# Kernel tuning notes

Measured on AMD Instinct MI355X. Metric: run time of the kernel, lower is better.

Reference implementation:

```python
import jax, jax.numpy as jnp
import numpy as np
import math

B, LQ, LK = 4, 512, 512
D_MODEL, NHEAD, NLABELS = 512, 8, 8
D_Q = D_MODEL // NHEAD


def setup_inputs() -> dict:
    key = jax.random.key(0)
    ks = jax.random.split(key, 12)
    xavier = lambda k, shape: jax.random.uniform(
        k, shape, jnp.float32,
        -math.sqrt(6.0 / (shape[0] + shape[1])), math.sqrt(6.0 / (shape[0] + shape[1])))
    return {
        "q": jax.random.normal(ks[0], (B, LQ, D_MODEL), jnp.float32),
        "k": jax.random.normal(ks[1], (B, LK, D_MODEL), jnp.float32),
        "edge_mask": jax.random.randint(ks[2], (B, LQ, LK, NLABELS), 0, 2).astype(jnp.float32),
        "padding_mask": jax.random.randint(ks[3], (B, LQ, LK), 0, 2).astype(jnp.float32),
        "w_q_w": xavier(ks[4], (D_MODEL, D_MODEL)),
        "w_q_b": jnp.zeros((D_MODEL,), jnp.float32),
        "w_k": xavier(ks[5], (D_MODEL, D_MODEL)),
        "w_v": xavier(ks[6], (D_MODEL, D_MODEL)),
        "w_h_w": xavier(ks[7], (D_MODEL, D_MODEL)),
        "w_h_b": jnp.zeros((D_MODEL,), jnp.float32),
        "b_ks": xavier(ks[8], (NLABELS, D_Q)),
        "b_vs": xavier(ks[9], (NLABELS, D_Q)),
    }


def reference(q, k, edge_mask, padding_mask, w_q_w, w_q_b, w_k, w_v, w_h_w, w_h_b, b_ks, b_vs):
    sz_b, len_q, _ = q.shape
    len_k = k.shape[1]
    temp = np.power(D_Q, 0.5).astype(np.float32)

    # projections -> (nhead, B, L, d_q), matching torch permute(2,0,1,3)
    query = (q @ w_q_w.T + w_q_b).reshape(sz_b, len_q, NHEAD, D_Q).transpose(2, 0, 1, 3)
    key = (k @ w_k.T).reshape(sz_b, len_k, NHEAD, D_Q).transpose(2, 0, 1, 3)
    value = (k @ w_v.T).reshape(sz_b, len_k, NHEAD, D_Q).transpose(2, 0, 1, 3)

    # content scores + relation-bias scores
    qk = jnp.einsum('hbqd,hbkd->hbqk', query, key)
    key_rel = jnp.einsum('bqkl,ld->bqkd', edge_mask, b_ks)      # (B,Lq,Lk,d_q)
    qkr = jnp.einsum('hbqd,bqkd->hbqk', query, key_rel)
    output_attention_weights = (qk + qkr) / temp                # pre-mask, as returned by torch

    # mask where no edge label AND padding_mask==1
    relation_mask = (edge_mask.sum(-1) + (1.0 - padding_mask)) == 0  # (B,Lq,Lk)
    rm = relation_mask[None, :, :, :]                                # broadcast over heads
    attn = jnp.where(rm, -jnp.inf, output_attention_weights)
    attn = jax.nn.softmax(attn, axis=-1)
    attn = jnp.where(rm, 0.0, attn)

    # value aggregation: content + relation values
    qv = jnp.einsum('hbqk,hbkd->hbqd', attn, value)
    val_rel = jnp.einsum('bqkl,ld->bqkd', edge_mask, b_vs)
    qvr = jnp.einsum('hbqk,bqkd->hbqd', attn, val_rel)

    out = (qv + qvr).transpose(1, 2, 0, 3).reshape(sz_b, len_q, D_MODEL)
    out = out @ w_h_w.T + w_h_b
    return out, output_attention_weights.reshape(NHEAD * sz_b, len_q, len_k)
```

## Files before the change

kernel.cpp:

```cpp
#include <hip/hip_runtime.h>
#include <math.h>

#define NB 4
#define LQ 512
#define LK 512
#define DM 512
#define NH 8
#define DQ 64
#define NL 8
#define QT 32
#define PSTR 520

typedef short bf16x8 __attribute__((ext_vector_type(8)));
typedef _Float16 f16x8 __attribute__((ext_vector_type(8)));
typedef _Float16 f16x2 __attribute__((ext_vector_type(2)));
typedef float f32x4 __attribute__((ext_vector_type(4)));

__device__ __forceinline__ unsigned short f2bf(float x) {
    unsigned u = __float_as_uint(x);
    u += 0x7fff + ((u >> 16) & 1);
    return (unsigned short)(u >> 16);
}
__device__ __forceinline__ float bf2f(unsigned x) {
    return __uint_as_float(x << 16);
}
__device__ __forceinline__ unsigned short f2h(float x) {
    _Float16 h = (_Float16)x;
    return __builtin_bit_cast(unsigned short, h);
}
__device__ __forceinline__ void gld16(const void* g, void* l) {
    __builtin_amdgcn_global_load_lds(
        (const __attribute__((address_space(1))) void*)g,
        (__attribute__((address_space(3))) void*)l, 16, 0, 0);
}

#define WAITVM(N) asm volatile("s_waitcnt vmcnt(" #N ")" ::: "memory")
#define LGKM0()   asm volatile("s_waitcnt lgkmcnt(0)" ::: "memory")
#define BARR()    do { asm volatile("" ::: "memory"); \
                       __builtin_amdgcn_s_barrier();  \
                       asm volatile("" ::: "memory"); } while (0)

__global__ __launch_bounds__(256) void prep_kernel(
        const float* __restrict__ q,  const float* __restrict__ k,
        const float* __restrict__ wq, const float* __restrict__ wk,
        const float* __restrict__ wv, const float* __restrict__ wh,
        const float* __restrict__ em, const float* __restrict__ pad,
        unsigned short* __restrict__ qb,  unsigned short* __restrict__ kb,
        unsigned short* __restrict__ wqb, unsigned short* __restrict__ wkb,
        unsigned short* __restrict__ wvb, unsigned short* __restrict__ whb,
        unsigned short* __restrict__ Pk) {
    const int tid = threadIdx.x;
    const int y = blockIdx.y;
    if (y < 6) {
        const float* s; unsigned short* d; int n;
        switch (y) {
            case 0: s = q;  d = qb;  n = NB * LQ * DM; break;
            case 1: s = k;  d = kb;  n = NB * LK * DM; break;
            case 2: s = wq; d = wqb; n = DM * DM; break;
            case 3: s = wk; d = wkb; n = DM * DM; break;
            case 4: s = wv; d = wvb; n = DM * DM; break;
            default: s = wh; d = whb; n = DM * DM; break;
        }
        const int i = blockIdx.x * 256 + tid;
        if (i * 8 >= n) return;
        const float4* sv = (const float4*)s;
        const float4 a = sv[2 * (size_t)i], b = sv[2 * (size_t)i + 1];
        uint4 o;
        o.x = (unsigned)f2bf(a.x) | ((unsigned)f2bf(a.y) << 16);
        o.y = (unsigned)f2bf(a.z) | ((unsigned)f2bf(a.w) << 16);
        o.z = (unsigned)f2bf(b.x) | ((unsigned)f2bf(b.y) << 16);
        o.w = (unsigned)f2bf(b.z) | ((unsigned)f2bf(b.w) << 16);
        *(uint4*)(d + (size_t)i * 8) = o;
    } else {
        const int row = blockIdx.x * 4 + (tid >> 6);
        const int k0 = (tid & 63) * 8;
        const float* eb = em + ((size_t)row * LK + k0) * NL;
        const float4 pv0 = *(const float4*)(pad + (size_t)row * LK + k0);
        const float4 pv1 = *(const float4*)(pad + (size_t)row * LK + k0 + 4);
        const float pv[8] = {pv0.x, pv0.y, pv0.z, pv0.w, pv1.x, pv1.y, pv1.z, pv1.w};
        unsigned short outv[8];
#pragma unroll
        for (int kk = 0; kk < 8; ++kk) {
            const float4 v0 = *(const float4*)(eb + kk * 8);
            const float4 v1 = *(const float4*)(eb + kk * 8 + 4);
            unsigned b_ = 0;
            b_ |= (v0.x != 0.f) << 0; b_ |= (v0.y != 0.f) << 1;
            b_ |= (v0.z != 0.f) << 2; b_ |= (v0.w != 0.f) << 3;
            b_ |= (v1.x != 0.f) << 4; b_ |= (v1.y != 0.f) << 5;
            b_ |= (v1.z != 0.f) << 6; b_ |= (v1.w != 0.f) << 7;
            b_ |= (pv[kk] != 0.f) << 8;
            outv[kk] = (unsigned short)b_;
        }
        uint4 o;
        o.x = (unsigned)outv[0] | ((unsigned)outv[1] << 16);
        o.y = (unsigned)outv[2] | ((unsigned)outv[3] << 16);
        o.z = (unsigned)outv[4] | ((unsigned)outv[5] << 16);
        o.w = (unsigned)outv[6] | ((unsigned)outv[7] << 16);
        *(uint4*)(Pk + (size_t)row * LK + k0) = o;
    }
}

__device__ __forceinline__ void gemm64core(const unsigned short* __restrict__ Ag, int lda,
                                           const unsigned short* __restrict__ Bg, int ldb,
                                           short* As, short* Bs,
                                           f32x4 (&acc)[2][2]) {
    const int tid = threadIdx.x;
    const int wave = tid >> 6, lane = tid & 63;
    const int quad = lane >> 4, l16 = lane & 15;
    const int wr = wave >> 1, wc = wave & 1;
    const int r_ = tid >> 2, c_ = (tid & 3) * 8;
    const unsigned short* Ar = Ag + (size_t)r_ * lda + c_;
    const unsigned short* Br = Bg + (size_t)r_ * ldb + c_;
    gld16(Ar, (char*)As + wave * 1024);
    gld16(Br, (char*)Bs + wave * 1024);
#pragma unroll
    for (int s = 0; s < 16; ++s) {
        if (s < 15) {
            const int nb = (s + 1) & 1;
            gld16(Ar + (s + 1) * 32, (char*)As + nb * 4096 + wave * 1024);
            gld16(Br + (s + 1) * 32, (char*)Bs + nb * 4096 + wave * 1024);
            WAITVM(2);
        } else {
            WAITVM(0);
        }
        BARR();
        const int cb = s & 1;
        bf16x8 af[2], bf[2];
#pragma unroll
        for (int i = 0; i < 2; ++i)
            af[i] = *(const bf16x8*)&As[cb * 2048 + (wr * 32 + i * 16 + l16) * 32 + quad * 8];
#pragma unroll
        for (int j = 0; j < 2; ++j)
            bf[j] = *(const bf16x8*)&Bs[cb * 2048 + (wc * 32 + j * 16 + l16) * 32 + quad * 8];
#pragma unroll
        for (int i = 0; i < 2; ++i)
#pragma unroll
            for (int j = 0; j < 2; ++j)
                acc[i][j] = __builtin_amdgcn_mfma_f32_16x16x32_bf16(af[i], bf[j], acc[i][j], 0, 0, 0);
        BARR();
    }
}

__global__ __launch_bounds__(256) void proj_all(const unsigned short* __restrict__ qb,
                                                const unsigned short* __restrict__ kb,
                                                const unsigned short* __restrict__ wqb,
                                                const unsigned short* __restrict__ wkb,
                                                const unsigned short* __restrict__ wvb,
                                                const float* __restrict__ w_q_b,
                                                unsigned short* __restrict__ Qp,
                                                unsigned short* __restrict__ Kp,
                                                unsigned short* __restrict__ Vt) {
    __shared__ __align__(16) short As[2][64 * 32];
    __shared__ __align__(16) short Bs[2][64 * 32];
    const unsigned short* A; const unsigned short* W; const float* bias;
    unsigned short* C; int mode;
    switch (blockIdx.z) {
        case 0:  A = qb; W = wqb; bias = w_q_b;  C = Qp; mode = 0; break;
        case 1:  A = kb; W = wkb; bias = nullptr; C = Kp; mode = 0; break;
        default: A = kb; W = wvb; bias = nullptr; C = Vt; mode = 1; break;
    }
    f32x4 acc[2][2];
    const f32x4 zz = {0.f, 0.f, 0.f, 0.f};
#pragma unroll
    for (int i = 0; i < 2; ++i)
#pragma unroll
        for (int j = 0; j < 2; ++j) acc[i][j] = zz;
    const int m0 = blockIdx.x * 64, n0 = blockIdx.y * 64;
    gemm64core(A + (size_t)m0 * DM, DM, W + (size_t)n0 * DM, DM, &As[0][0], &Bs[0][0], acc);
    const int tid = threadIdx.x, wave = tid >> 6, lane = tid & 63;
    const int quad = lane >> 4, l16 = lane & 15;
    const int wr = wave >> 1, wc = wave & 1;
#pragma unroll
    for (int i = 0; i < 2; ++i)
#pragma unroll
        for (int r = 0; r < 4; ++r) {
            const int gm = m0 + wr * 32 + i * 16 + quad * 4 + r;
#pragma unroll
            for (int j = 0; j < 2; ++j) {
                const int gn = n0 + wc * 32 + j * 16 + l16;
                float v = acc[i][j][r];
                if (bias) v += bias[gn];
                if (mode == 0) C[(size_t)gm * DM + gn] = f2bf(v);
                else C[(size_t)(gm >> 9) * (DM * LK) + (size_t)gn * LK + (gm & 511)] = f2h(v);
            }
        }
}

#define STAGE_K(c, hb) do {                                                       \
    _Pragma("unroll")                                                             \
    for (int it_ = 0; it_ < 2; ++it_) {                                           \
        const int e_ = it_ * 512 + tid;                                           \
        const int kr_ = e_ >> 3, ch_ = e_ & 7;                                    \
        gld16(Kp + (size_t)(b * LK + (c) * 128 + kr_) * DM + h * DQ               \
                  + ((ch_ ^ (kr_ & 7)) * 8),                                      \
              (char*)&Kc[hb][0] + it_ * 8192 + wave * 1024);                      \
    } } while (0)

#define STAGE_V(vc, hb) do {                                                      \
    _Pragma("unroll")                                                             \
    for (int it_ = 0; it_ < 2; ++it_) {                                           \
        const int e_ = it_ * 512 + tid;                                           \
        const int dd_ = e_ >> 4, ch_ = e_ & 15;                                   \
        gld16(Vt + (size_t)(b * DM + h * DQ + dd_) * LK + (vc) * 128              \
                  + ((ch_ ^ (dd_ & 15)) * 8),                                     \
              (char*)&Kc[hb][0] + it_ * 8192 + wave * 1024);                      \
    } } while (0)

#define COMPUTE_K(c, hb) do {                                                     \
    _Pragma("unroll")                                                             \
    for (int kdi_ = 0; kdi_ < 2; ++kdi_) {                                        \
        const int krow_ = wave * 16 + l16;                                        \
        const int kch_ = (kdi_ * 4 + quad) ^ (krow_ & 7);                         \
        const bf16x8 bfv_ = *(const bf16x8*)&Kc[hb][krow_ * 64 + kch_ * 8];       \
        acc[c][0] = __builtin_amdgcn_mfma_f32_16x16x32_bf16(qf[0][kdi_], bfv_,    \
                                                            acc[c][0], 0, 0, 0); \
        acc[c][1] = __builtin_amdgcn_mfma_f32_16x16x32_bf16(qf[1][kdi_], bfv_,    \
                                                            acc[c][1], 0, 0, 0); \
    } } while (0)

#define COMPUTE_V(vc, hb) do {                                                    \
    _Pragma("unroll")                                                             \
    for (int kd_ = 0; kd_ < 128; kd_ += 32) {                                     \
        const int vrow_ = ni * 16 + l16;                                          \
        const int vch_ = ((kd_ >> 3) + quad) ^ (vrow_ & 15);                      \
        const f16x8 afv_ = *(const f16x8*)&Ps[(mi * 16 + l16) * PSTR              \
                                              + (vc) * 128 + kd_ + quad * 8];     \
        const f16x8 bfv_ = *(const f16x8*)&Kc[hb][vrow_ * 128 + vch_ * 8];        \
        oacc = __builtin_amdgcn_mfma_f32_16x16x32_f16(afv_, bfv_, oacc, 0, 0, 0); \
    } } while (0)

__global__ __launch_bounds__(512, 4) void attn_fused(
        const unsigned short* __restrict__ Qp,
        const unsigned short* __restrict__ Kp,
        const unsigned short* __restrict__ Vt,
        const unsigned short* __restrict__ Pk,
        const float* __restrict__ b_ks,
        const float* __restrict__ b_vs,
        float* __restrict__ weights,
        unsigned short* __restrict__ Hb) {
    __shared__ __align__(16) short Qs[QT * 64];
    __shared__ __align__(16) short Kc[2][128 * 64];
    __shared__ __align__(16) short Ps[QT * PSTR];
    __shared__ float svS[QT * NL];
    __shared__ float lutS[QT * 32];
    __shared__ float tS[QT * NL];
    __shared__ float redA[QT * 8];
    __shared__ float redB[QT * 8];

    const int tid = threadIdx.x, wave = tid >> 6, lane = tid & 63;
    const int quad = lane >> 4, l16 = lane & 15;
    const int q0 = blockIdx.x * QT;
    const int z = blockIdx.y, h = z >> 2, b = z & 3;

    const int srow = tid >> 4, sl = (tid >> 1) & 7, shalf = tid & 1;
    bf16x8 sq[4];
    {
        const unsigned short* qrow = Qp + (size_t)(b * LQ + q0 + srow) * DM + h * DQ + shalf * 32;
#pragma unroll
        for (int d0 = 0; d0 < 4; ++d0) sq[d0] = *(const bf16x8*)&qrow[d0 * 8];
    }

    if (tid < 256) {
        const int row = tid >> 3, ch = tid & 7;
        gld16(Qp + (size_t)(b * LQ + q0 + row) * DM + h * DQ + ((ch ^ (row & 7)) * 8),
              (char*)Qs + wave * 1024);
    }
    STAGE_K(0, 0);
    STAGE_K(1, 1);

    {
        const float* bk = b_ks + sl * DQ + shalf * 32;
        float s = 0.f;
#pragma unroll
        for (int d0 = 0; d0 < 4; ++d0)
#pragma unroll
            for (int j = 0; j < 8; ++j)
                s = fmaf(bf2f((unsigned short)sq[d0][j]), bk[d0 * 8 + j], s);
        s += __shfl_xor(s, 1, 64);
        if (shalf == 0) svS[srow * 8 + sl] = s;
    }

    f32x4 acc[4][2];
    const f32x4 zz = {0.f, 0.f, 0.f, 0.f};
#pragma unroll
    for (int c = 0; c < 4; ++c) { acc[c][0] = zz; acc[c][1] = zz; }
    bf16x8 qf[2][2];

    WAITVM(2); LGKM0(); BARR();
#pragma unroll
    for (int i = 0; i < 2; ++i)
#pragma unroll
        for (int kdi = 0; kdi < 2; ++kdi)
            qf[i][kdi] = *(const bf16x8*)&Qs[(i * 16 + l16) * 64
                                             + (((kdi * 4) + quad) ^ (l16 & 7)) * 8];
#pragma unroll
    for (int e2 = 0; e2 < 2; ++e2) {
        const int e = e2 * 512 + tid;
        const int row = e >> 5, idx = e & 31;
        const float* sp = &svS[row * 8 + ((idx & 16) ? 4 : 0)];
        float v = 0.f;
        v += (idx & 1) ? sp[0] : 0.f;
        v += (idx & 2) ? sp[1] : 0.f;
        v += (idx & 4) ? sp[2] : 0.f;
        v += (idx & 8) ? sp[3] : 0.f;
        lutS[e] = v;
    }
    COMPUTE_K(0, 0);
    LGKM0(); BARR();
    STAGE_K(2, 0);
    WAITVM(2); LGKM0(); BARR();
    COMPUTE_K(1, 1);
    LGKM0(); BARR();
    STAGE_K(3, 1);
    WAITVM(2); LGKM0(); BARR();
    COMPUTE_K(2, 0);
    LGKM0(); BARR();
    STAGE_V(0, 0);
    WAITVM(2); LGKM0(); BARR();
    COMPUTE_K(3, 1);
    LGKM0(); BARR();
    STAGE_V(1, 1);

#pragma unroll
    for (int i = 0; i < 2; ++i)
#pragma unroll
        for (int r = 0; r < 4; ++r) {
            const int row = i * 16 + quad * 4 + r;
            const int gq = q0 + row;
            const float* lrow = &lutS[row * 32];
            const unsigned short* prow = Pk + (size_t)(b * LQ + gq) * LK;
            float* wrow = weights + ((size_t)z * LQ + gq) * LK;
            float pm = -__builtin_inff();
#pragma unroll
            for (int c = 0; c < 4; ++c) {
                const int col = c * 128 + wave * 16 + l16;
                const unsigned w_ = prow[col];
                const float rel = lrow[w_ & 15u] + lrow[16 + ((w_ >> 4) & 15u)];
                const float wv = (acc[c][i][r] + rel) * 0.125f;
                wrow[col] = wv;
                const float m = ((w_ & 0x1FFu) == 0x100u) ? -__builtin_inff() : wv;
                acc[c][i][r] = m;
                pm = fmaxf(pm, m);
            }
#pragma unroll
            for (int o = 1; o < 16; o <<= 1) pm = fmaxf(pm, __shfl_xor(pm, o, 64));
            float ps = 0.f;
#pragma unroll
            for (int c = 0; c < 4; ++c) {
                const float e = __expf(acc[c][i][r] - pm);
                acc[c][i][r] = e;
                ps += e;
            }
#pragma unroll
            for (int o = 1; o < 16; o <<= 1) ps += __shfl_xor(ps, o, 64);
            if (l16 == 0) { redA[row * 8 + wave] = pm; redB[row * 8 + wave] = ps; }
        }
    LGKM0(); BARR();

#pragma unroll
    for (int i = 0; i < 2; ++i)
#pragma unroll
        for (int r = 0; r < 4; ++r) {
            const int row = i * 16 + quad * 4 + r;
            const f32x4 pa = *(const f32x4*)&redA[row * 8];
            const f32x4 pb = *(const f32x4*)&redA[row * 8 + 4];
            const f32x4 sa = *(const f32x4*)&redB[row * 8];
            const f32x4 sb = *(const f32x4*)&redB[row * 8 + 4];
            const float M = fmaxf(fmaxf(fmaxf(pa[0], pa[1]), fmaxf(pa[2], pa[3])),
                                  fmaxf(fmaxf(pb[0], pb[1]), fmaxf(pb[2], pb[3])));
            const float S = sa[0] * __expf(pa[0] - M) + sa[1] * __expf(pa[1] - M)
                          + sa[2] * __expf(pa[2] - M) + sa[3] * __expf(pa[3] - M)
                          + sb[0] * __expf(pb[0] - M) + sb[1] * __expf(pb[1] - M)
                          + sb[2] * __expf(pb[2] - M) + sb[3] * __expf(pb[3] - M);
            const float own = redA[row * 8 + wave];
            const float alpha = __expf(own - M) / S;
#pragma unroll
            for (int c = 0; c < 4; ++c) {
                const int col = c * 128 + wave * 16 + l16;
                Ps[row * PSTR + col] = (short)f2h(acc[c][i][r] * alpha);
            }
        }
    LGKM0(); BARR();

    {
        const int row = tid >> 4, l = (tid >> 1) & 7, half = tid & 1;
        const uint4* pw = (const uint4*)(Pk + (size_t)(b * LQ + q0 + row) * LK + half * 256);
        const uint4* aw = (const uint4*)&Ps[row * PSTR + half * 256];
        float tv = 0.f;
#pragma unroll 4
        for (int kk = 0; kk < 32; ++kk) {
            const uint4 wb = pw[kk];
            const uint4 av = aw[kk];
            const unsigned w4[4] = {wb.x, wb.y, wb.z, wb.w};
            const unsigned a4[4] = {av.x, av.y, av.z, av.w};
            f16x2 hacc = {(_Float16)0.f, (_Float16)0.f};
#pragma unroll
            for (int u = 0; u < 4; ++u) {
                const unsigned bits = (w4[u] >> l) & 0x10001u;
                const unsigned msk = bits * 0x3c00u;
                hacc += __builtin_bit_cast(f16x2, a4[u]) * __builtin_bit_cast(f16x2, msk);
            }
            tv += (float)hacc[0] + (float)hacc[1];
        }
        tv += __shfl_xor(tv, 1, 64);
        if (half == 0) tS[row * 8 + l] = tv;
    }

    f32x4 oacc = zz;
    const int mi = wave & 1, ni = wave >> 1;
    WAITVM(0); LGKM0(); BARR();
    COMPUTE_V(0, 0);
    BARR();
    STAGE_V(2, 0);
    WAITVM(2); LGKM0(); BARR();
    COMPUTE_V(1, 1);
    BARR();
    STAGE_V(3, 1);
    WAITVM(2); LGKM0(); BARR();
    COMPUTE_V(2, 0);
    WAITVM(0); LGKM0(); BARR();
    COMPUTE_V(3, 1);

    const int gd = ni * 16 + l16;
    float bvv[NL];
#pragma unroll
    for (int l = 0; l < NL; ++l) bvv[l] = b_vs[l * DQ + gd];
#pragma unroll
    for (int r = 0; r < 4; ++r) {
        const int row = mi * 16 + quad * 4 + r;
        const float* tp = &tS[row * 8];
        float o = oacc[r];
#pragma unroll
        for (int l = 0; l < NL; ++l) o = fmaf(tp[l], bvv[l], o);
        Hb[(size_t)(b * LQ + q0 + row) * DM + h * DQ + gd] = f2bf(o);
    }
}

__global__ __launch_bounds__(256) void outproj_mfma(const unsigned short* __restrict__ Hb,
                                                    const unsigned short* __restrict__ whb,
                                                    const float* __restrict__ bias,
                                                    float* __restrict__ C) {
    __shared__ __align__(16) short As[2][64 * 32];
    __shared__ __align__(16) short Bs[2][64 * 32];
    f32x4 acc[2][2];
    const f32x4 zz = {0.f, 0.f, 0.f, 0.f};
#pragma unroll
    for (int i = 0; i < 2; ++i)
#pragma unroll
        for (int j = 0; j < 2; ++j) acc[i][j] = zz;
    const int m0 = blockIdx.x * 64, n0 = blockIdx.y * 64;
    gemm64core(Hb + (size_t)m0 * DM, DM, whb + (size_t)n0 * DM, DM, &As[0][0], &Bs[0][0], acc);
    const int tid = threadIdx.x, wave = tid >> 6, lane = tid & 63;
    const int quad = lane >> 4, l16 = lane & 15;
    const int wr = wave >> 1, wc = wave & 1;
#pragma unroll
    for (int i = 0; i < 2; ++i)
#pragma unroll
        for (int r = 0; r < 4; ++r) {
            const int gm = m0 + wr * 32 + i * 16 + quad * 4 + r;
#pragma unroll
            for (int j = 0; j < 2; ++j) {
                const int gn = n0 + wc * 32 + j * 16 + l16;
                C[(size_t)gm * DM + gn] = acc[i][j][r] + bias[gn];
            }
        }
}

extern "C" void kernel_launch(void* const* d_in, const int* in_sizes, int n_in,
                              void* d_out, int out_size, void* d_ws, size_t ws_size,
                              hipStream_t stream) {
    const float* q     = (const float*)d_in[0];
    const float* k     = (const float*)d_in[1];
    const float* em    = (const float*)d_in[2];
    const float* pad   = (const float*)d_in[3];
    const float* w_q_w = (const float*)d_in[4];
    const float* w_q_b = (const float*)d_in[5];
    const float* w_k   = (const float*)d_in[6];
    const float* w_v   = (const float*)d_in[7];
    const float* w_h_w = (const float*)d_in[8];
    const float* w_h_b = (const float*)d_in[9];
    const float* b_ks  = (const float*)d_in[10];
    const float* b_vs  = (const float*)d_in[11];

    float* out     = (float*)d_out;
    float* weights = out + (size_t)NB * LQ * DM;

    char* ws = (char*)d_ws;
    unsigned short* qb  = (unsigned short*)(ws + 0);
    unsigned short* kb  = (unsigned short*)(ws + 2097152);
    unsigned short* wqb = (unsigned short*)(ws + 4194304);
    unsigned short* wkb = (unsigned short*)(ws + 4718592);
    unsigned short* wvb = (unsigned short*)(ws + 5242880);
    unsigned short* whb = (unsigned short*)(ws + 5767168);
    unsigned short* Qp  = (unsigned short*)(ws + 6291456);
    unsigned short* Kp  = (unsigned short*)(ws + 8388608);
    unsigned short* Vt  = (unsigned short*)(ws + 10485760);
    unsigned short* Hb  = (unsigned short*)(ws + 12582912);
    unsigned short* Pk  = (unsigned short*)(ws + 14680064);

    prep_kernel<<<dim3(512, 7), 256, 0, stream>>>(q, k, w_q_w, w_k, w_v, w_h_w,
                                                  em, pad, qb, kb, wqb, wkb, wvb, whb, Pk);
    proj_all<<<dim3(32, 8, 3), 256, 0, stream>>>(qb, kb, wqb, wkb, wvb, w_q_b, Qp, Kp, Vt);
    attn_fused<<<dim3(LQ / QT, 32), 512, 0, stream>>>(Qp, Kp, Vt, Pk, b_ks, b_vs, weights, Hb);
    outproj_mfma<<<dim3(32, 8), 256, 0, stream>>>(Hb, whb, w_h_b, out);
}
```

Measured before the change: 166.6 us.

## Fuse fp32-to-bf16 conversion into projection GEMMs and merge prep into front kernel

Removes the separate prep kernel that converted q, k and the weights to bf16. The projection and output GEMMs now stage fp32 tiles directly into swizzled LDS and convert to bf16 with packed convert instructions while building fragments. Edge/padding mask packing moves into an extra z-slice of the projection launch, so there is one fewer launch and no bf16 intermediate round-trip through global memory. In exchange the GEMMs load twice the bytes per tile into LDS and do conversion work inside the inner loop.

```diff
diff --git a/kernel.cpp b/kernel.cpp
--- a/kernel.cpp
+++ b/kernel.cpp
@@ -15,6 +15,7 @@
 typedef _Float16 f16x8 __attribute__((ext_vector_type(8)));
 typedef _Float16 f16x2 __attribute__((ext_vector_type(2)));
 typedef float f32x4 __attribute__((ext_vector_type(4)));
+typedef unsigned u32x4 __attribute__((ext_vector_type(4)));
 
 __device__ __forceinline__ unsigned short f2bf(float x) {
     unsigned u = __float_as_uint(x);
@@ -40,98 +41,101 @@
                        __builtin_amdgcn_s_barrier();  \
                        asm volatile("" ::: "memory"); } while (0)
 
-__global__ __launch_bounds__(256) void prep_kernel(
-        const float* __restrict__ q,  const float* __restrict__ k,
-        const float* __restrict__ wq, const float* __restrict__ wk,
-        const float* __restrict__ wv, const float* __restrict__ wh,
-        const float* __restrict__ em, const float* __restrict__ pad,
-        unsigned short* __restrict__ qb,  unsigned short* __restrict__ kb,
-        unsigned short* __restrict__ wqb, unsigned short* __restrict__ wkb,
-        unsigned short* __restrict__ wvb, unsigned short* __restrict__ whb,
-        unsigned short* __restrict__ Pk) {
-    const int tid = threadIdx.x;
-    const int y = blockIdx.y;
-    if (y < 6) {
-        const float* s; unsigned short* d; int n;
-        switch (y) {
-            case 0: s = q;  d = qb;  n = NB * LQ * DM; break;
-            case 1: s = k;  d = kb;  n = NB * LK * DM; break;
-            case 2: s = wq; d = wqb; n = DM * DM; break;
-            case 3: s = wk; d = wkb; n = DM * DM; break;
-            case 4: s = wv; d = wvb; n = DM * DM; break;
-            default: s = wh; d = whb; n = DM * DM; break;
-        }
-        const int i = blockIdx.x * 256 + tid;
-        if (i * 8 >= n) return;
-        const float4* sv = (const float4*)s;
-        const float4 a = sv[2 * (size_t)i], b = sv[2 * (size_t)i + 1];
-        uint4 o;
-        o.x = (unsigned)f2bf(a.x) | ((unsigned)f2bf(a.y) << 16);
-        o.y = (unsigned)f2bf(a.z) | ((unsigned)f2bf(a.w) << 16);
-        o.z = (unsigned)f2bf(b.x) | ((unsigned)f2bf(b.y) << 16);
-        o.w = (unsigned)f2bf(b.z) | ((unsigned)f2bf(b.w) << 16);
-        *(uint4*)(d + (size_t)i * 8) = o;
-    } else {
-        const int row = blockIdx.x * 4 + (tid >> 6);
-        const int k0 = (tid & 63) * 8;
-        const float* eb = em + ((size_t)row * LK + k0) * NL;
-        const float4 pv0 = *(const float4*)(pad + (size_t)row * LK + k0);
-        const float4 pv1 = *(const float4*)(pad + (size_t)row * LK + k0 + 4);
-        const float pv[8] = {pv0.x, pv0.y, pv0.z, pv0.w, pv1.x, pv1.y, pv1.z, pv1.w};
-        unsigned short outv[8];
-#pragma unroll
-        for (int kk = 0; kk < 8; ++kk) {
-            const float4 v0 = *(const float4*)(eb + kk * 8);
-            const float4 v1 = *(const float4*)(eb + kk * 8 + 4);
-            unsigned b_ = 0;
-            b_ |= (v0.x != 0.f) << 0; b_ |= (v0.y != 0.f) << 1;
-            b_ |= (v0.z != 0.f) << 2; b_ |= (v0.w != 0.f) << 3;
-            b_ |= (v1.x != 0.f) << 4; b_ |= (v1.y != 0.f) << 5;
-            b_ |= (v1.z != 0.f) << 6; b_ |= (v1.w != 0.f) << 7;
-            b_ |= (pv[kk] != 0.f) << 8;
-            outv[kk] = (unsigned short)b_;
-        }
-        uint4 o;
-        o.x = (unsigned)outv[0] | ((unsigned)outv[1] << 16);
-        o.y = (unsigned)outv[2] | ((unsigned)outv[3] << 16);
-        o.z = (unsigned)outv[4] | ((unsigned)outv[5] << 16);
-        o.w = (unsigned)outv[6] | ((unsigned)outv[7] << 16);
-        *(uint4*)(Pk + (size_t)row * LK + k0) = o;
-    }
-}
-
-__device__ __forceinline__ void gemm64core(const unsigned short* __restrict__ Ag, int lda,
-                                           const unsigned short* __restrict__ Bg, int ldb,
-                                           short* As, short* Bs,
-                                           f32x4 (&acc)[2][2]) {
+__device__ __forceinline__ bf16x8 pk_bf16x8(f32x4 a, f32x4 b) {
+    unsigned r0, r1, r2, r3;
+    asm("v_cvt_pk_bf16_f32 %0, %1, %2" : "=v"(r0) : "v"(a[0]), "v"(a[1]));
+    asm("v_cvt_pk_bf16_f32 %0, %1, %2" : "=v"(r1) : "v"(a[2]), "v"(a[3]));
+    asm("v_cvt_pk_bf16_f32 %0, %1, %2" : "=v"(r2) : "v"(b[0]), "v"(b[1]));
+    asm("v_cvt_pk_bf16_f32 %0, %1, %2" : "=v"(r3) : "v"(b[2]), "v"(b[3]));
+    const u32x4 u = {r0, r1, r2, r3};
+    return __builtin_bit_cast(bf16x8, u);
+}
+
+#define STG_FF(Mg, base, k0) do {                                          \
+    _Pragma("unroll")                                                      \
+    for (int it_ = 0; it_ < 2; ++it_) {                                    \
+        const int t_ = it_ * 256 + tid;                                    \
+        const int row_ = t_ >> 3, sl_ = t_ & 7;                            \
+        const int gch_ = sl_ ^ (row_ & 7);                                 \
+        gld16((Mg) + (size_t)row_ * DM + (k0) + gch_ * 4,                  \
+              (char*)(base) + it_ * 4096 + wave * 1024);                   \
+    } } while (0)
+
+__device__ __forceinline__ bf16x8 ldfrag_f32(const float* Mf, int row, int quad) {
+    const int s0 = (2 * quad) ^ (row & 7), s1 = (2 * quad + 1) ^ (row & 7);
+    const f32x4 lo = *(const f32x4*)&Mf[row * 32 + s0 * 4];
+    const f32x4 hi = *(const f32x4*)&Mf[row * 32 + s1 * 4];
+    return pk_bf16x8(lo, hi);
+}
+
+__device__ __forceinline__ void pack_pk(const float* __restrict__ em,
+                                        const float* __restrict__ pad,
+                                        unsigned short* __restrict__ Pk,
+                                        int row, int k0) {
+    const float* eb = em + ((size_t)row * LK + k0) * NL;
+    const float4 pv0 = *(const float4*)(pad + (size_t)row * LK + k0);
+    const float4 pv1 = *(const float4*)(pad + (size_t)row * LK + k0 + 4);
+    const float pv[8] = {pv0.x, pv0.y, pv0.z, pv0.w, pv1.x, pv1.y, pv1.z, pv1.w};
+    unsigned short outv[8];
+#pragma unroll
+    for (int kk = 0; kk < 8; ++kk) {
+        const float4 v0 = *(const float4*)(eb + kk * 8);
+        const float4 v1 = *(const float4*)(eb + kk * 8 + 4);
+        unsigned b_ = 0;
+        b_ |= (v0.x != 0.f) << 0; b_ |= (v0.y != 0.f) << 1;
+        b_ |= (v0.z != 0.f) << 2; b_ |= (v0.w != 0.f) << 3;
+        b_ |= (v1.x != 0.f) << 4; b_ |= (v1.y != 0.f) << 5;
+        b_ |= (v1.z != 0.f) << 6; b_ |= (v1.w != 0.f) << 7;
+        b_ |= (pv[kk] != 0.f) << 8;
+        outv[kk] = (unsigned short)b_;
+    }
+    uint4 o;
+    o.x = (unsigned)outv[0] | ((unsigned)outv[1] << 16);
+    o.y = (unsigned)outv[2] | ((unsigned)outv[3] << 16);
+    o.z = (unsigned)outv[4] | ((unsigned)outv[5] << 16);
+    o.w = (unsigned)outv[6] | ((unsigned)outv[7] << 16);
+    *(uint4*)(Pk + (size_t)row * LK + k0) = o;
+}
+
+template<int MODE>
+__device__ void gemm_ff(const float* __restrict__ Ag,
+                        const float* __restrict__ Bg,
+                        const float* __restrict__ bias,
+                        unsigned short* __restrict__ Cp,
+                        int m0, int n0, float* As, float* Bs) {
     const int tid = threadIdx.x;
     const int wave = tid >> 6, lane = tid & 63;
     const int quad = lane >> 4, l16 = lane & 15;
     const int wr = wave >> 1, wc = wave & 1;
-    const int r_ = tid >> 2, c_ = (tid & 3) * 8;
-    const unsigned short* Ar = Ag + (size_t)r_ * lda + c_;
-    const unsigned short* Br = Bg + (size_t)r_ * ldb + c_;
-    gld16(Ar, (char*)As + wave * 1024);
-    gld16(Br, (char*)Bs + wave * 1024);
+    f32x4 acc[2][2];
+    const f32x4 zz = {0.f, 0.f, 0.f, 0.f};
+#pragma unroll
+    for (int i = 0; i < 2; ++i)
+#pragma unroll
+        for (int j = 0; j < 2; ++j) acc[i][j] = zz;
+    STG_FF(Ag, (char*)As, 0);
+    STG_FF(Bg, (char*)Bs, 0);
 #pragma unroll
     for (int s = 0; s < 16; ++s) {
         if (s < 15) {
             const int nb = (s + 1) & 1;
-            gld16(Ar + (s + 1) * 32, (char*)As + nb * 4096 + wave * 1024);
-            gld16(Br + (s + 1) * 32, (char*)Bs + nb * 4096 + wave * 1024);
-            WAITVM(2);
+            STG_FF(Ag, (char*)As + nb * 8192, (s + 1) * 32);
+            STG_FF(Bg, (char*)Bs + nb * 8192, (s + 1) * 32);
+            WAITVM(4);
         } else {
             WAITVM(0);
         }
         BARR();
         const int cb = s & 1;
+        const float* Af = As + cb * 2048;
+        const float* Bf = Bs + cb * 2048;
         bf16x8 af[2], bf[2];
 #pragma unroll
         for (int i = 0; i < 2; ++i)
-            af[i] = *(const bf16x8*)&As[cb * 2048 + (wr * 32 + i * 16 + l16) * 32 + quad * 8];
+            af[i] = ldfrag_f32(Af, wr * 32 + i * 16 + l16, quad);
 #pragma unroll
         for (int j = 0; j < 2; ++j)
-            bf[j] = *(const bf16x8*)&Bs[cb * 2048 + (wc * 32 + j * 16 + l16) * 32 + quad * 8];
+            bf[j] = ldfrag_f32(Bf, wc * 32 + j * 16 + l16, quad);
 #pragma unroll
         for (int i = 0; i < 2; ++i)
 #pragma unroll
@@ -139,37 +143,6 @@
                 acc[i][j] = __builtin_amdgcn_mfma_f32_16x16x32_bf16(af[i], bf[j], acc[i][j], 0, 0, 0);
         BARR();
     }
-}
-
-__global__ __launch_bounds__(256) void proj_all(const unsigned short* __restrict__ qb,
-                                                const unsigned short* __restrict__ kb,
-                                                const unsigned short* __restrict__ wqb,
-                                                const unsigned short* __restrict__ wkb,
-                                                const unsigned short* __restrict__ wvb,
-                                                const float* __restrict__ w_q_b,
-                                                unsigned short* __restrict__ Qp,
-                                                unsigned short* __restrict__ Kp,
-                                                unsigned short* __restrict__ Vt) {
-    __shared__ __align__(16) short As[2][64 * 32];
-    __shared__ __align__(16) short Bs[2][64 * 32];
-    const unsigned short* A; const unsigned short* W; const float* bias;
-    unsigned short* C; int mode;
-    switch (blockIdx.z) {
-        case 0:  A = qb; W = wqb; bias = w_q_b;  C = Qp; mode = 0; break;
-        case 1:  A = kb; W = wkb; bias = nullptr; C = Kp; mode = 0; break;
-        default: A = kb; W = wvb; bias = nullptr; C = Vt; mode = 1; break;
-    }
-    f32x4 acc[2][2];
-    const f32x4 zz = {0.f, 0.f, 0.f, 0.f};
-#pragma unroll
-    for (int i = 0; i < 2; ++i)
-#pragma unroll
-        for (int j = 0; j < 2; ++j) acc[i][j] = zz;
-    const int m0 = blockIdx.x * 64, n0 = blockIdx.y * 64;
-    gemm64core(A + (size_t)m0 * DM, DM, W + (size_t)n0 * DM, DM, &As[0][0], &Bs[0][0], acc);
-    const int tid = threadIdx.x, wave = tid >> 6, lane = tid & 63;
-    const int quad = lane >> 4, l16 = lane & 15;
-    const int wr = wave >> 1, wc = wave & 1;
 #pragma unroll
     for (int i = 0; i < 2; ++i)
 #pragma unroll
@@ -179,11 +152,45 @@
             for (int j = 0; j < 2; ++j) {
                 const int gn = n0 + wc * 32 + j * 16 + l16;
                 float v = acc[i][j][r];
-                if (bias) v += bias[gn];
-                if (mode == 0) C[(size_t)gm * DM + gn] = f2bf(v);
-                else C[(size_t)(gm >> 9) * (DM * LK) + (size_t)gn * LK + (gm & 511)] = f2h(v);
+                if (MODE == 0) {
+                    if (bias) v += bias[gn];
+                    Cp[(size_t)gm * DM + gn] = f2bf(v);
+                } else {
+                    Cp[(size_t)(gm >> 9) * (DM * LK) + (size_t)gn * LK + (gm & 511)] = f2h(v);
+                }
             }
         }
+}
+
+__global__ __launch_bounds__(256) void front(
+        const float* __restrict__ q,  const float* __restrict__ k,
+        const float* __restrict__ wq, const float* __restrict__ wk,
+        const float* __restrict__ wv, const float* __restrict__ w_q_b,
+        const float* __restrict__ em, const float* __restrict__ pad,
+        unsigned short* __restrict__ Qp, unsigned short* __restrict__ Kp,
+        unsigned short* __restrict__ Vt, unsigned short* __restrict__ Pk) {
+    const int tid = threadIdx.x;
+    if (blockIdx.z == 3) {
+        const int blk = blockIdx.y * 32 + blockIdx.x;
+#pragma unroll
+        for (int p = 0; p < 2; ++p) {
+            const int row = blk * 8 + p * 4 + (tid >> 6);
+            pack_pk(em, pad, Pk, row, (tid & 63) * 8);
+        }
+        return;
+    }
+    __shared__ __align__(16) float As[2][2048];
+    __shared__ __align__(16) float Bs[2][2048];
+    const int m0 = blockIdx.x * 64, n0 = blockIdx.y * 64;
+    if (blockIdx.z == 0)
+        gemm_ff<0>(q + (size_t)m0 * DM, wq + (size_t)n0 * DM, w_q_b, Qp, m0, n0,
+                   &As[0][0], &Bs[0][0]);
+    else if (blockIdx.z == 1)
+        gemm_ff<0>(k + (size_t)m0 * DM, wk + (size_t)n0 * DM, nullptr, Kp, m0, n0,
+                   &As[0][0], &Bs[0][0]);
+    else
+        gemm_ff<1>(k + (size_t)m0 * DM, wv + (size_t)n0 * DM, nullptr, Vt, m0, n0,
+                   &As[0][0], &Bs[0][0]);
 }
 
 #define STAGE_K(c, hb) do {                                                       \
@@ -193,7 +200,7 @@
         const int kr_ = e_ >> 3, ch_ = e_ & 7;                                    \
         gld16(Kp + (size_t)(b * LK + (c) * 128 + kr_) * DM + h * DQ               \
                   + ((ch_ ^ (kr_ & 7)) * 8),                                      \
-              (char*)&Kc[hb][0] + it_ * 8192 + wave * 1024);                      \
+              (char*)(&Kc[hb][0]) + it_ * 8192 + wave * 1024);                    \
     } } while (0)
 
 #define STAGE_V(vc, hb) do {                                                      \
@@ -203,7 +210,7 @@
         const int dd_ = e_ >> 4, ch_ = e_ & 15;                                   \
         gld16(Vt + (size_t)(b * DM + h * DQ + dd_) * LK + (vc) * 128              \
                   + ((ch_ ^ (dd_ & 15)) * 8),                                     \
-              (char*)&Kc[hb][0] + it_ * 8192 + wave * 1024);                      \
+              (char*)(&Kc[hb][0]) + it_ * 8192 + wave * 1024);                    \
     } } while (0)
 
 #define COMPUTE_K(c, hb) do {                                                     \
@@ -436,23 +443,54 @@
     }
 }
 
-__global__ __launch_bounds__(256) void outproj_mfma(const unsigned short* __restrict__ Hb,
-                                                    const unsigned short* __restrict__ whb,
-                                                    const float* __restrict__ bias,
-                                                    float* __restrict__ C) {
-    __shared__ __align__(16) short As[2][64 * 32];
-    __shared__ __align__(16) short Bs[2][64 * 32];
+__global__ __launch_bounds__(256) void outproj(const unsigned short* __restrict__ Hb,
+                                               const float* __restrict__ wh,
+                                               const float* __restrict__ bias,
+                                               float* __restrict__ C) {
+    __shared__ __align__(16) short As[2][2048];
+    __shared__ __align__(16) float Bs[2][2048];
+    const int tid = threadIdx.x;
+    const int wave = tid >> 6, lane = tid & 63;
+    const int quad = lane >> 4, l16 = lane & 15;
+    const int wr = wave >> 1, wc = wave & 1;
+    const int m0 = blockIdx.x * 64, n0 = blockIdx.y * 64;
     f32x4 acc[2][2];
     const f32x4 zz = {0.f, 0.f, 0.f, 0.f};
 #pragma unroll
     for (int i = 0; i < 2; ++i)
 #pragma unroll
         for (int j = 0; j < 2; ++j) acc[i][j] = zz;
-    const int m0 = blockIdx.x * 64, n0 = blockIdx.y * 64;
-    gemm64core(Hb + (size_t)m0 * DM, DM, whb + (size_t)n0 * DM, DM, &As[0][0], &Bs[0][0], acc);
-    const int tid = threadIdx.x, wave = tid >> 6, lane = tid & 63;
-    const int quad = lane >> 4, l16 = lane & 15;
-    const int wr = wave >> 1, wc = wave & 1;
+    const unsigned short* Arp = Hb + (size_t)(m0 + (tid >> 2)) * DM + (tid & 3) * 8;
+    const float* Bgp = wh + (size_t)n0 * DM;
+    gld16(Arp, (char*)As + wave * 1024);
+    STG_FF(Bgp, (char*)Bs, 0);
+#pragma unroll
+    for (int s = 0; s < 16; ++s) {
+        if (s < 15) {
+            const int nb = (s + 1) & 1;
+            gld16(Arp + (s + 1) * 32, (char*)As + nb * 4096 + wave * 1024);
+            STG_FF(Bgp, (char*)Bs + nb * 8192, (s + 1) * 32);
+            WAITVM(3);
+        } else {
+            WAITVM(0);
+        }
+        BARR();
+        const int cb = s & 1;
+        const float* Bf = &Bs[0][0] + cb * 2048;
+        bf16x8 af[2], bf[2];
+#pragma unroll
+        for (int i = 0; i < 2; ++i)
+            af[i] = *(const bf16x8*)&As[cb][(wr * 32 + i * 16 + l16) * 32 + quad * 8];
+#pragma unroll
+        for (int j = 0; j < 2; ++j)
+            bf[j] = ldfrag_f32(Bf, wc * 32 + j * 16 + l16, quad);
+#pragma unroll
+        for (int i = 0; i < 2; ++i)
+#pragma unroll
+            for (int j = 0; j < 2; ++j)
+                acc[i][j] = __builtin_amdgcn_mfma_f32_16x16x32_bf16(af[i], bf[j], acc[i][j], 0, 0, 0);
+        BARR();
+    }
 #pragma unroll
     for (int i = 0; i < 2; ++i)
 #pragma unroll
@@ -486,21 +524,14 @@
     float* weights = out + (size_t)NB * LQ * DM;
 
     char* ws = (char*)d_ws;
-    unsigned short* qb  = (unsigned short*)(ws + 0);
-    unsigned short* kb  = (unsigned short*)(ws + 2097152);
-    unsigned short* wqb = (unsigned short*)(ws + 4194304);
-    unsigned short* wkb = (unsigned short*)(ws + 4718592);
-    unsigned short* wvb = (unsigned short*)(ws + 5242880);
-    unsigned short* whb = (unsigned short*)(ws + 5767168);
-    unsigned short* Qp  = (unsigned short*)(ws + 6291456);
-    unsigned short* Kp  = (unsigned short*)(ws + 8388608);
-    unsigned short* Vt  = (unsigned short*)(ws + 10485760);
-    unsigned short* Hb  = (unsigned short*)(ws + 12582912);
-    unsigned short* Pk  = (unsigned short*)(ws + 14680064);
-
-    prep_kernel<<<dim3(512, 7), 256, 0, stream>>>(q, k, w_q_w, w_k, w_v, w_h_w,
-                                                  em, pad, qb, kb, wqb, wkb, wvb, whb, Pk);
-    proj_all<<<dim3(32, 8, 3), 256, 0, stream>>>(qb, kb, wqb, wkb, wvb, w_q_b, Qp, Kp, Vt);
+    unsigned short* Qp = (unsigned short*)(ws + 0);
+    unsigned short* Kp = (unsigned short*)(ws + 2097152);
+    unsigned short* Vt = (unsigned short*)(ws + 4194304);
+    unsigned short* Hb = (unsigned short*)(ws + 6291456);
+    unsigned short* Pk = (unsigned short*)(ws + 8388608);
+
+    front<<<dim3(32, 8, 4), 256, 0, stream>>>(q, k, w_q_w, w_k, w_v, w_q_b,
+                                              em, pad, Qp, Kp, Vt, Pk);
     attn_fused<<<dim3(LQ / QT, 32), 512, 0, stream>>>(Qp, Kp, Vt, Pk, b_ks, b_vs, weights, Hb);
-    outproj_mfma<<<dim3(32, 8), 256, 0, stream>>>(Hb, whb, w_h_b, out);
-}
+    outproj<<<dim3(32, 8), 256, 0, stream>>>(Hb, w_h_w, w_h_b, out);
+}
```

After: 164.1 us. No clear change (-1.5%).
